# Performance work log

Hardware: AMD Instinct MI355X
Metric: run time of the kernel (lower is better)

## Reference

```python
import jax, jax.numpy as jnp
import numpy as np

WS = 8          # window_size
DISP = WS // 2  # cyclic shift displacement
HEADS = 12
HEAD_DIM = 32
SCALE = HEAD_DIM ** -0.5


def _rel_indices():
    # indices of (x, y) for x in range(WS) for y in range(WS)
    idx = np.stack(np.meshgrid(np.arange(WS), np.arange(WS), indexing='ij'), -1).reshape(-1, 2)
    return idx[None, :, :] - idx[:, None, :] + WS - 1  # (WS^2, WS^2, 2), values in [0, 2*WS-2]


def _masks():
    ninf = -np.inf
    # upper/lower mask: blocks attention across the vertical wrap boundary
    m_ul = np.zeros((WS * WS, WS * WS), np.float32)
    m_ul[-DISP * WS:, :-DISP * WS] = ninf
    m_ul[:-DISP * WS, -DISP * WS:] = ninf
    # left/right mask: blocks attention across the horizontal wrap boundary
    m4 = np.zeros((WS, WS, WS, WS), np.float32)  # (h1, w1, h2, w2)
    m4[:, -DISP:, :, :-DISP] = ninf
    m4[:, :-DISP, :, -DISP:] = ninf
    m_lr = m4.reshape(WS * WS, WS * WS)
    return jnp.asarray(m_ul), jnp.asarray(m_lr)


def setup_inputs() -> dict:
    key = jax.random.key(0)
    k1, k2, k3, k4, k5 = jax.random.split(key, 5)
    dim = HEADS * HEAD_DIM  # 384
    return {
        'x': jax.random.normal(k1, (16, 64, 64, dim), jnp.float32),
        'w_qkv': jax.random.normal(k2, (dim, 3 * dim), jnp.float32) * 0.02,
        'pos_embedding': jax.random.normal(k3, (2 * WS - 1, 2 * WS - 1), jnp.float32),
        'w_out': jax.random.normal(k4, (dim, dim), jnp.float32) * 0.02,
        'b_out': jax.random.normal(k5, (dim,), jnp.float32) * 0.02,
    }


def reference(x, w_qkv, pos_embedding, w_out, b_out):
    b, H, W, dim = x.shape
    nw_h, nw_w = H // WS, W // WS
    # cyclic shift
    x = jnp.roll(x, (-DISP, -DISP), axis=(1, 2))
    qkv = x @ w_qkv  # (b, H, W, 3*inner)

    def to_windows(t):
        # (b, H, W, inner) -> (b, heads, nw_h*nw_w, WS*WS, head_dim)
        t = t.reshape(b, nw_h, WS, nw_w, WS, HEADS, HEAD_DIM)
        return t.transpose(0, 5, 1, 3, 2, 4, 6).reshape(b, HEADS, nw_h * nw_w, WS * WS, HEAD_DIM)

    q, k, v = [to_windows(t) for t in jnp.split(qkv, 3, axis=-1)]
    dots = jnp.einsum('bhwid,bhwjd->bhwij', q, k) * SCALE

    rel = _rel_indices()
    dots = dots + pos_embedding[rel[..., 0], rel[..., 1]]  # relative position bias

    m_ul, m_lr = _masks()
    dots = dots.at[:, :, -nw_w:].add(m_ul)            # last row of windows
    dots = dots.at[:, :, nw_w - 1::nw_w].add(m_lr)    # last column of windows

    attn = jax.nn.softmax(dots, axis=-1)
    out = jnp.einsum('bhwij,bhwjd->bhwid', attn, v)
    # windows -> image layout
    out = out.reshape(b, HEADS, nw_h, nw_w, WS, WS, HEAD_DIM)
    out = out.transpose(0, 2, 4, 3, 5, 1, 6).reshape(b, H, W, HEADS * HEAD_DIM)
    out = out @ w_out + b_out
    # cyclic back shift
    return jnp.roll(out, (DISP, DISP), axis=(1, 2))
```

## Files before the change

### kernel.cpp

```cpp
#include <hip/hip_runtime.h>
#include <stdint.h>

#define HEADS 12
#define HD 32
#define DIM 384
#define NQKV 1152
#define NPIX 4096
#define NB 16

typedef __attribute__((ext_vector_type(8))) short bf16x8;
typedef __attribute__((ext_vector_type(4))) short bf16x4;
typedef __attribute__((ext_vector_type(4))) float f32x4;

__device__ __forceinline__ unsigned short f2bf(float f) {
  uint32_t u = __builtin_bit_cast(uint32_t, f);
  u += 0x7FFF + ((u >> 16) & 1);
  return (unsigned short)(u >> 16);
}

#define GL_LDS(gp, lp) __builtin_amdgcn_global_load_lds( \
    (const __attribute__((address_space(1))) void*)(gp),  \
    (__attribute__((address_space(3))) void*)(lp), 16, 0, 0)

__global__ void convert_all(const float* __restrict__ x,
                            const float* __restrict__ wqkv,
                            const float* __restrict__ wout,
                            unsigned short* __restrict__ xb,
                            unsigned short* __restrict__ wqkvT,
                            unsigned short* __restrict__ woutT) {
  int bid = blockIdx.x;
  if (bid < 12288) {
    int i = bid * 256 + threadIdx.x;
    const float4* xp = (const float4*)x;
    float4 a = xp[2 * i], b2 = xp[2 * i + 1];
    union { bf16x8 v; unsigned short s[8]; } u;
    u.s[0] = f2bf(a.x);  u.s[1] = f2bf(a.y);
    u.s[2] = f2bf(a.z);  u.s[3] = f2bf(a.w);
    u.s[4] = f2bf(b2.x); u.s[5] = f2bf(b2.y);
    u.s[6] = f2bf(b2.z); u.s[7] = f2bf(b2.w);
    ((bf16x8*)xb)[i] = u.v;
  } else {
    int tid = (bid - 12288) * 256 + threadIdx.x;
    if (tid < NQKV * DIM) {
      int n = tid / DIM, k = tid % DIM;
      wqkvT[tid] = f2bf(wqkv[(size_t)k * NQKV + n]);
    }
    if (tid < DIM * DIM) {
      int n = tid / DIM, k = tid % DIM;
      woutT[tid] = f2bf(wout[(size_t)k * DIM + n]);
    }
  }
}

__global__ __launch_bounds__(256, 4) void gemm_qkv(
    const unsigned short* __restrict__ xb,
    const unsigned short* __restrict__ wT,
    unsigned short* __restrict__ qkv)
{
  __shared__ unsigned short lA[128 * 64];
  __shared__ unsigned short lB[128 * 64];
  const int tid = threadIdx.x;
  const int wid = tid >> 6, lane = tid & 63;
  const int wr = wid >> 1, wc = wid & 1;
  const int lr = lane >> 4, lc = lane & 15;

  const int f = blockIdx.x;
  const int xcd = f & 7, idx = f >> 3;
  const int nt = idx % 9, mt = xcd * 64 + idx / 9;
  const int m0 = mt * 128, n0 = nt * 128;

  const int srow = wid * 32 + (lane >> 3);
  const int scol = ((lane & 7) ^ (lane >> 3)) * 8;
  const unsigned short* agp = xb + (size_t)(m0 + srow) * DIM + scol;
  const unsigned short* bgp = wT + (size_t)(n0 + srow) * DIM + scol;

  const f32x4 z4 = {0.f, 0.f, 0.f, 0.f};
  f32x4 acc[4][4];
#pragma unroll
  for (int i = 0; i < 4; i++)
#pragma unroll
    for (int j = 0; j < 4; j++) acc[i][j] = z4;

  auto stage = [&](int t) {
#pragma unroll
    for (int i = 0; i < 4; i++) {
      GL_LDS(agp + (size_t)(i * 8) * DIM + t * 64, &lA[(wid * 4 + i) * 512]);
      GL_LDS(bgp + (size_t)(i * 8) * DIM + t * 64, &lB[(wid * 4 + i) * 512]);
    }
  };
  auto compute = [&]() {
    const int sw = lc & 7;
#pragma unroll
    for (int kk = 0; kk < 2; kk++) {
      bf16x8 afr[4], bfr[4];
#pragma unroll
      for (int mi = 0; mi < 4; mi++)
        afr[mi] = *(const bf16x8*)&lA[(wr * 64 + mi * 16 + lc) * 64 + (((kk * 4 + lr) ^ sw) * 8)];
#pragma unroll
      for (int ni = 0; ni < 4; ni++)
        bfr[ni] = *(const bf16x8*)&lB[(wc * 64 + ni * 16 + lc) * 64 + (((kk * 4 + lr) ^ sw) * 8)];
#pragma unroll
      for (int mi = 0; mi < 4; mi++)
#pragma unroll
        for (int ni = 0; ni < 4; ni++)
          acc[mi][ni] = __builtin_amdgcn_mfma_f32_16x16x32_bf16(afr[mi], bfr[ni], acc[mi][ni], 0, 0, 0);
    }
  };

  for (int t = 0; t < 6; ++t) {
    stage(t);
    __syncthreads();
    compute();
    if (t < 5) __syncthreads();
  }

#pragma unroll
  for (int mi = 0; mi < 4; mi++) {
    int row = m0 + wr * 64 + mi * 16 + lr * 4;
#pragma unroll
    for (int reg = 0; reg < 4; reg++) {
      size_t rb = (size_t)(row + reg) * NQKV + n0 + wc * 64 + lc;
#pragma unroll
      for (int ni = 0; ni < 4; ni++)
        qkv[rb + ni * 16] = f2bf(acc[mi][ni][reg]);
    }
  }
}

__global__ __launch_bounds__(256) void attn_kernel(
    const unsigned short* __restrict__ qkv,
    const float* __restrict__ pos,
    unsigned short* __restrict__ Z)
{
  __shared__ float s_pos[225];
  __shared__ unsigned short Plds[4][64 * 80];
  __shared__ unsigned short Vt[4][32 * 80];

  if (threadIdx.x < 225) s_pos[threadIdx.x] = pos[threadIdx.x];

  const int wid = threadIdx.x >> 6, lane = threadIdx.x & 63;
  const int lr = lane >> 4, lc = lane & 15;
  const int task = blockIdx.x * 4 + wid;
  const int win = task & 63;
  const int head = (task >> 6) % HEADS;
  const int b = task / (HEADS * 64);
  const int wh = win >> 3, ww = win & 7;
  const bool ulm = (wh == 7), lrm = (ww == 7);

  auto pixof = [&](int t) {
    int hh = (wh * 8 + (t >> 3) + 4) & 63;
    int w2 = (ww * 8 + (t & 7) + 4) & 63;
    return hh * 64 + w2;
  };

  bf16x8 qf[4], kf[4];
  unsigned short* vt = &Vt[wid][0];
#pragma unroll
  for (int g = 0; g < 4; ++g) {
    int t = g * 16 + lc;
    const unsigned short* base =
        qkv + (size_t)(b * NPIX + pixof(t)) * NQKV + head * HD + lr * 8;
    qf[g] = *(const bf16x8*)(base);
    kf[g] = *(const bf16x8*)(base + DIM);
    union { bf16x8 v; unsigned short s[8]; } uv;
    uv.v = *(const bf16x8*)(base + 2 * DIM);
#pragma unroll
    for (int j = 0; j < 8; j++) vt[(lr * 8 + j) * 80 + t] = uv.s[j];
  }
  __syncthreads();

  const f32x4 z4 = {0.f, 0.f, 0.f, 0.f};
  f32x4 sacc[4][4];
#pragma unroll
  for (int i = 0; i < 4; i++)
#pragma unroll
    for (int j = 0; j < 4; j++) sacc[i][j] = z4;

#pragma unroll
  for (int mi = 0; mi < 4; mi++)
#pragma unroll
    for (int ni = 0; ni < 4; ni++)
      sacc[mi][ni] = __builtin_amdgcn_mfma_f32_16x16x32_bf16(qf[mi], kf[ni], sacc[mi][ni], 0, 0, 0);

  const float SC = 0.17677669529663687f;
#pragma unroll
  for (int mi = 0; mi < 4; mi++) {
#pragma unroll
    for (int reg = 0; reg < 4; reg++) {
      int i = mi * 16 + lr * 4 + reg;
      int xi = i >> 3, yi = i & 7;
#pragma unroll
      for (int ni = 0; ni < 4; ni++) {
        int j = ni * 16 + lc;
        int xj = j >> 3, yj = j & 7;
        float s = sacc[mi][ni][reg] * SC + s_pos[(xj - xi + 7) * 15 + (yj - yi + 7)];
        if (ulm && ((i >= 32) != (j >= 32))) s = -1e30f;
        if (lrm && ((yi >= 4) != (yj >= 4))) s = -1e30f;
        sacc[mi][ni][reg] = s;
      }
    }
  }

  float inv[4][4];
  unsigned short* pl = &Plds[wid][0];
#pragma unroll
  for (int mi = 0; mi < 4; mi++) {
#pragma unroll
    for (int reg = 0; reg < 4; reg++) {
      float m = fmaxf(fmaxf(sacc[mi][0][reg], sacc[mi][1][reg]),
                      fmaxf(sacc[mi][2][reg], sacc[mi][3][reg]));
      m = fmaxf(m, __shfl_xor(m, 1));
      m = fmaxf(m, __shfl_xor(m, 2));
      m = fmaxf(m, __shfl_xor(m, 4));
      m = fmaxf(m, __shfl_xor(m, 8));
      int i = mi * 16 + lr * 4 + reg;
      float sum = 0.f;
#pragma unroll
      for (int ni = 0; ni < 4; ni++) {
        float p = exp2f((sacc[mi][ni][reg] - m) * 1.44269504f);
        sum += p;
        pl[i * 80 + ni * 16 + lc] = f2bf(p);
      }
      sum += __shfl_xor(sum, 1);
      sum += __shfl_xor(sum, 2);
      sum += __shfl_xor(sum, 4);
      sum += __shfl_xor(sum, 8);
      inv[mi][reg] = 1.0f / sum;
    }
  }
  __syncthreads();

  f32x4 oacc[4][2];
#pragma unroll
  for (int i = 0; i < 4; i++) { oacc[i][0] = z4; oacc[i][1] = z4; }

#pragma unroll
  for (int kk = 0; kk < 2; kk++) {
    bf16x8 vfr[2];
#pragma unroll
    for (int ni = 0; ni < 2; ni++)
      vfr[ni] = *(const bf16x8*)&vt[(ni * 16 + lc) * 80 + kk * 32 + lr * 8];
#pragma unroll
    for (int mi = 0; mi < 4; mi++) {
      bf16x8 pf = *(const bf16x8*)&pl[(mi * 16 + lc) * 80 + kk * 32 + lr * 8];
#pragma unroll
      for (int ni = 0; ni < 2; ni++)
        oacc[mi][ni] = __builtin_amdgcn_mfma_f32_16x16x32_bf16(pf, vfr[ni], oacc[mi][ni], 0, 0, 0);
    }
  }

#pragma unroll
  for (int mi = 0; mi < 4; mi++) {
#pragma unroll
    for (int reg = 0; reg < 4; reg++) {
      int i = mi * 16 + lr * 4 + reg;
      size_t zb = ((size_t)b * NPIX + pixof(i)) * DIM + head * HD;
      float sc = inv[mi][reg];
#pragma unroll
      for (int ni = 0; ni < 2; ni++)
        Z[zb + ni * 16 + lc] = f2bf(oacc[mi][ni][reg] * sc);
    }
  }
}

__global__ __launch_bounds__(256, 4) void gemm_out(
    const unsigned short* __restrict__ Zb,
    const unsigned short* __restrict__ wT,
    const float* __restrict__ bout,
    float* __restrict__ out)
{
  __shared__ unsigned short lA[128 * 64];
  __shared__ unsigned short lB[128 * 64];
  const int tid = threadIdx.x;
  const int wid = tid >> 6, lane = tid & 63;
  const int wr = wid >> 1, wc = wid & 1;
  const int lr = lane >> 4, lc = lane & 15;

  const int f = blockIdx.x;
  const int xcd = f & 7, idx = f >> 3;
  const int nt = idx % 3, mt = xcd * 64 + idx / 3;
  const int m0 = mt * 128, n0 = nt * 128;

  const int srow = wid * 32 + (lane >> 3);
  const int scol = ((lane & 7) ^ (lane >> 3)) * 8;
  const unsigned short* agp = Zb + (size_t)(m0 + srow) * DIM + scol;
  const unsigned short* bgp = wT + (size_t)(n0 + srow) * DIM + scol;

  const f32x4 z4 = {0.f, 0.f, 0.f, 0.f};
  f32x4 acc[4][4];
#pragma unroll
  for (int i = 0; i < 4; i++)
#pragma unroll
    for (int j = 0; j < 4; j++) acc[i][j] = z4;

  auto stage = [&](int t) {
#pragma unroll
    for (int i = 0; i < 4; i++) {
      GL_LDS(agp + (size_t)(i * 8) * DIM + t * 64, &lA[(wid * 4 + i) * 512]);
      GL_LDS(bgp + (size_t)(i * 8) * DIM + t * 64, &lB[(wid * 4 + i) * 512]);
    }
  };
  auto compute = [&]() {
    const int sw = lc & 7;
#pragma unroll
    for (int kk = 0; kk < 2; kk++) {
      bf16x8 afr[4], bfr[4];
#pragma unroll
      for (int mi = 0; mi < 4; mi++)
        afr[mi] = *(const bf16x8*)&lA[(wr * 64 + mi * 16 + lc) * 64 + (((kk * 4 + lr) ^ sw) * 8)];
#pragma unroll
      for (int ni = 0; ni < 4; ni++)
        bfr[ni] = *(const bf16x8*)&lB[(wc * 64 + ni * 16 + lc) * 64 + (((kk * 4 + lr) ^ sw) * 8)];
#pragma unroll
      for (int mi = 0; mi < 4; mi++)
#pragma unroll
        for (int ni = 0; ni < 4; ni++)
          acc[mi][ni] = __builtin_amdgcn_mfma_f32_16x16x32_bf16(afr[mi], bfr[ni], acc[mi][ni], 0, 0, 0);
    }
  };

  for (int t = 0; t < 6; ++t) {
    stage(t);
    __syncthreads();
    compute();
    if (t < 5) __syncthreads();
  }

  float bo[4];
#pragma unroll
  for (int ni = 0; ni < 4; ni++) bo[ni] = bout[n0 + wc * 64 + ni * 16 + lc];

#pragma unroll
  for (int mi = 0; mi < 4; mi++) {
    int row = m0 + wr * 64 + mi * 16 + lr * 4;
#pragma unroll
    for (int reg = 0; reg < 4; reg++) {
      size_t rb = (size_t)(row + reg) * DIM + n0 + wc * 64 + lc;
#pragma unroll
      for (int ni = 0; ni < 4; ni++)
        out[rb + ni * 16] = acc[mi][ni][reg] + bo[ni];
    }
  }
}

extern "C" void kernel_launch(void* const* d_in, const int* in_sizes, int n_in,
                              void* d_out, int out_size, void* d_ws, size_t ws_size,
                              hipStream_t stream) {
  const float* x    = (const float*)d_in[0];
  const float* wqkv = (const float*)d_in[1];
  const float* pos  = (const float*)d_in[2];
  const float* wout = (const float*)d_in[3];
  const float* bout = (const float*)d_in[4];
  float* out = (float*)d_out;

  char* ws = (char*)d_ws;
  unsigned short* wqkvT = (unsigned short*)ws;
  unsigned short* woutT = (unsigned short*)(ws + 884736);
  unsigned short* qkv   = (unsigned short*)(ws + 1179648);
  unsigned short* xb    = (unsigned short*)(ws + 1179648 + 150994944);
  unsigned short* Zb    = xb;

  convert_all<<<14016, 256, 0, stream>>>(x, wqkv, wout, xb, wqkvT, woutT);
  gemm_qkv<<<4608, 256, 0, stream>>>(xb, wqkvT, qkv);
  attn_kernel<<<3072, 256, 0, stream>>>(qkv, pos, Zb);
  gemm_out<<<1536, 256, 0, stream>>>(Zb, woutT, bout, out);
}
```

Baseline: 192.9 us.

## Precompute bias/mask table and keep softmax probabilities in registers via transposed QK

Adds a precomputed table of four variants (64x64 each) of relative-position bias plus shift masks, built in the convert kernel and stored temporarily in the output buffer. The attention kernel loads bias rows directly instead of computing indices and masks per element. It computes S^T = K·Q^T so each lane's probabilities can be normalized, packed to bf16 and reshuffled with ds_bpermute into MFMA operand layout. This removes the P round-trip through LDS and both barriers. V^T in LDS gets an XOR swizzle to reduce bank conflicts. It relies on gemm_out overwriting the table region later and adds cross-lane permute traffic.

```diff
diff --git a/kernel.cpp b/kernel.cpp
--- a/kernel.cpp
+++ b/kernel.cpp
@@ -25,9 +25,11 @@
 __global__ void convert_all(const float* __restrict__ x,
                             const float* __restrict__ wqkv,
                             const float* __restrict__ wout,
+                            const float* __restrict__ pos,
                             unsigned short* __restrict__ xb,
                             unsigned short* __restrict__ wqkvT,
-                            unsigned short* __restrict__ woutT) {
+                            unsigned short* __restrict__ woutT,
+                            float* __restrict__ tab) {
   int bid = blockIdx.x;
   if (bid < 12288) {
     int i = bid * 256 + threadIdx.x;
@@ -39,7 +41,7 @@
     u.s[4] = f2bf(b2.x); u.s[5] = f2bf(b2.y);
     u.s[6] = f2bf(b2.z); u.s[7] = f2bf(b2.w);
     ((bf16x8*)xb)[i] = u.v;
-  } else {
+  } else if (bid < 14016) {
     int tid = (bid - 12288) * 256 + threadIdx.x;
     if (tid < NQKV * DIM) {
       int n = tid / DIM, k = tid % DIM;
@@ -49,6 +51,15 @@
       int n = tid / DIM, k = tid % DIM;
       woutT[tid] = f2bf(wout[(size_t)k * DIM + n]);
     }
+  } else {
+    int tid = (bid - 14016) * 256 + threadIdx.x;
+    int v = tid >> 12, rem = tid & 4095;
+    int i = rem >> 6, j = rem & 63;
+    int xi = i >> 3, yi = i & 7, xj = j >> 3, yj = j & 7;
+    float val = pos[(xj - xi + 7) * 15 + (yj - yi + 7)];
+    if ((v & 1) && ((i >= 32) != (j >= 32))) val = -1e30f;
+    if ((v & 2) && ((yi >= 4) != (yj >= 4))) val = -1e30f;
+    tab[tid] = val;
   }
 }
 
@@ -129,14 +140,10 @@
 
 __global__ __launch_bounds__(256) void attn_kernel(
     const unsigned short* __restrict__ qkv,
-    const float* __restrict__ pos,
+    const float* __restrict__ tab,
     unsigned short* __restrict__ Z)
 {
-  __shared__ float s_pos[225];
-  __shared__ unsigned short Plds[4][64 * 80];
   __shared__ unsigned short Vt[4][32 * 80];
-
-  if (threadIdx.x < 225) s_pos[threadIdx.x] = pos[threadIdx.x];
 
   const int wid = threadIdx.x >> 6, lane = threadIdx.x & 63;
   const int lr = lane >> 4, lc = lane & 15;
@@ -145,7 +152,7 @@
   const int head = (task >> 6) % HEADS;
   const int b = task / (HEADS * 64);
   const int wh = win >> 3, ww = win & 7;
-  const bool ulm = (wh == 7), lrm = (ww == 7);
+  const float* tv = tab + (((wh == 7) ? 1 : 0) + ((ww == 7) ? 2 : 0)) * 4096;
 
   auto pixof = [&](int t) {
     int hh = (wh * 8 + (t >> 3) + 4) & 63;
@@ -153,8 +160,8 @@
     return hh * 64 + w2;
   };
 
+  unsigned short* vt = &Vt[wid][0];
   bf16x8 qf[4], kf[4];
-  unsigned short* vt = &Vt[wid][0];
 #pragma unroll
   for (int g = 0; g < 4; ++g) {
     int t = g * 16 + lc;
@@ -165,70 +172,77 @@
     union { bf16x8 v; unsigned short s[8]; } uv;
     uv.v = *(const bf16x8*)(base + 2 * DIM);
 #pragma unroll
-    for (int j = 0; j < 8; j++) vt[(lr * 8 + j) * 80 + t] = uv.s[j];
-  }
-  __syncthreads();
-
+    for (int j = 0; j < 8; j++) {
+      int row = lr * 8 + j;
+      int addr = row * 80 + (((g * 2 + (lc >> 3)) ^ ((row >> 2) & 3)) << 3) + (lc & 7);
+      vt[addr] = uv.s[j];
+    }
+  }
+
+  const float SC = 0.17677669529663687f;
   const f32x4 z4 = {0.f, 0.f, 0.f, 0.f};
-  f32x4 sacc[4][4];
-#pragma unroll
-  for (int i = 0; i < 4; i++)
-#pragma unroll
-    for (int j = 0; j < 4; j++) sacc[i][j] = z4;
-
-#pragma unroll
-  for (int mi = 0; mi < 4; mi++)
-#pragma unroll
-    for (int ni = 0; ni < 4; ni++)
-      sacc[mi][ni] = __builtin_amdgcn_mfma_f32_16x16x32_bf16(qf[mi], kf[ni], sacc[mi][ni], 0, 0, 0);
-
-  const float SC = 0.17677669529663687f;
-#pragma unroll
-  for (int mi = 0; mi < 4; mi++) {
-#pragma unroll
-    for (int reg = 0; reg < 4; reg++) {
-      int i = mi * 16 + lr * 4 + reg;
-      int xi = i >> 3, yi = i & 7;
-#pragma unroll
-      for (int ni = 0; ni < 4; ni++) {
-        int j = ni * 16 + lc;
-        int xj = j >> 3, yj = j & 7;
-        float s = sacc[mi][ni][reg] * SC + s_pos[(xj - xi + 7) * 15 + (yj - yi + 7)];
-        if (ulm && ((i >= 32) != (j >= 32))) s = -1e30f;
-        if (lrm && ((yi >= 4) != (yj >= 4))) s = -1e30f;
-        sacc[mi][ni][reg] = s;
+  uint32_t pf[4][2][4];
+  const int srcA = (lc + 16 * (2 * (lr & 1))) << 2;
+  const int srcB = srcA + 64;
+  const bool hiSel = (lr >> 1) != 0;
+
+#pragma unroll
+  for (int bq = 0; bq < 4; bq++) {
+    f32x4 tb[4];
+#pragma unroll
+    for (int a = 0; a < 4; a++)
+      tb[a] = *(const f32x4*)&tv[(bq * 16 + lc) * 64 + a * 16 + lr * 4];
+    f32x4 s[4];
+#pragma unroll
+    for (int a = 0; a < 4; a++)
+      s[a] = __builtin_amdgcn_mfma_f32_16x16x32_bf16(kf[a], qf[bq], z4, 0, 0, 0);
+
+    float m = -3.0e38f;
+#pragma unroll
+    for (int a = 0; a < 4; a++)
+#pragma unroll
+      for (int r = 0; r < 4; r++) {
+        float val = s[a][r] * SC + tb[a][r];
+        s[a][r] = val;
+        m = fmaxf(m, val);
       }
-    }
-  }
-
-  float inv[4][4];
-  unsigned short* pl = &Plds[wid][0];
-#pragma unroll
-  for (int mi = 0; mi < 4; mi++) {
-#pragma unroll
-    for (int reg = 0; reg < 4; reg++) {
-      float m = fmaxf(fmaxf(sacc[mi][0][reg], sacc[mi][1][reg]),
-                      fmaxf(sacc[mi][2][reg], sacc[mi][3][reg]));
-      m = fmaxf(m, __shfl_xor(m, 1));
-      m = fmaxf(m, __shfl_xor(m, 2));
-      m = fmaxf(m, __shfl_xor(m, 4));
-      m = fmaxf(m, __shfl_xor(m, 8));
-      int i = mi * 16 + lr * 4 + reg;
-      float sum = 0.f;
-#pragma unroll
-      for (int ni = 0; ni < 4; ni++) {
-        float p = exp2f((sacc[mi][ni][reg] - m) * 1.44269504f);
+    m = fmaxf(m, __shfl_xor(m, 16));
+    m = fmaxf(m, __shfl_xor(m, 32));
+    float sum = 0.f;
+#pragma unroll
+    for (int a = 0; a < 4; a++)
+#pragma unroll
+      for (int r = 0; r < 4; r++) {
+        float p = exp2f((s[a][r] - m) * 1.44269504f);
+        s[a][r] = p;
         sum += p;
-        pl[i * 80 + ni * 16 + lc] = f2bf(p);
       }
-      sum += __shfl_xor(sum, 1);
-      sum += __shfl_xor(sum, 2);
-      sum += __shfl_xor(sum, 4);
-      sum += __shfl_xor(sum, 8);
-      inv[mi][reg] = 1.0f / sum;
-    }
-  }
-  __syncthreads();
+    sum += __shfl_xor(sum, 16);
+    sum += __shfl_xor(sum, 32);
+    float iv = 1.0f / sum;
+
+    uint32_t pk[4][2];
+#pragma unroll
+    for (int a = 0; a < 4; a++)
+#pragma unroll
+      for (int w = 0; w < 2; w++) {
+        float plo = s[a][2 * w] * iv, phi = s[a][2 * w + 1] * iv;
+        uint32_t r;
+        asm("v_cvt_pk_bf16_f32 %0, %1, %2" : "=v"(r) : "v"(plo), "v"(phi));
+        pk[a][w] = r;
+      }
+#pragma unroll
+    for (int kk = 0; kk < 2; kk++)
+#pragma unroll
+      for (int wp = 0; wp < 4; wp++) {
+        int sa = (wp >> 1) ? srcB : srcA;
+        uint32_t lo = (uint32_t)__builtin_amdgcn_ds_bpermute(sa, (int)pk[2 * kk][wp & 1]);
+        uint32_t hi = (uint32_t)__builtin_amdgcn_ds_bpermute(sa, (int)pk[2 * kk + 1][wp & 1]);
+        pf[bq][kk][wp] = hiSel ? hi : lo;
+      }
+  }
+
+  asm volatile("s_waitcnt lgkmcnt(0)" ::: "memory");
 
   f32x4 oacc[4][2];
 #pragma unroll
@@ -238,14 +252,19 @@
   for (int kk = 0; kk < 2; kk++) {
     bf16x8 vfr[2];
 #pragma unroll
-    for (int ni = 0; ni < 2; ni++)
-      vfr[ni] = *(const bf16x8*)&vt[(ni * 16 + lc) * 80 + kk * 32 + lr * 8];
+    for (int dt = 0; dt < 2; dt++) {
+      int rowd = dt * 16 + lc;
+      int addr = rowd * 80 + ((((kk * 4 + lr) ^ (lc >> 2)) & 7) << 3);
+      vfr[dt] = *(const bf16x8*)&vt[addr];
+    }
 #pragma unroll
     for (int mi = 0; mi < 4; mi++) {
-      bf16x8 pf = *(const bf16x8*)&pl[(mi * 16 + lc) * 80 + kk * 32 + lr * 8];
-#pragma unroll
-      for (int ni = 0; ni < 2; ni++)
-        oacc[mi][ni] = __builtin_amdgcn_mfma_f32_16x16x32_bf16(pf, vfr[ni], oacc[mi][ni], 0, 0, 0);
+      union { uint32_t u[4]; bf16x8 v; } pu;
+      pu.u[0] = pf[mi][kk][0]; pu.u[1] = pf[mi][kk][1];
+      pu.u[2] = pf[mi][kk][2]; pu.u[3] = pf[mi][kk][3];
+#pragma unroll
+      for (int dt = 0; dt < 2; dt++)
+        oacc[mi][dt] = __builtin_amdgcn_mfma_f32_16x16x32_bf16(pu.v, vfr[dt], oacc[mi][dt], 0, 0, 0);
     }
   }
 
@@ -255,10 +274,9 @@
     for (int reg = 0; reg < 4; reg++) {
       int i = mi * 16 + lr * 4 + reg;
       size_t zb = ((size_t)b * NPIX + pixof(i)) * DIM + head * HD;
-      float sc = inv[mi][reg];
-#pragma unroll
-      for (int ni = 0; ni < 2; ni++)
-        Z[zb + ni * 16 + lc] = f2bf(oacc[mi][ni][reg] * sc);
+#pragma unroll
+      for (int dt = 0; dt < 2; dt++)
+        Z[zb + dt * 16 + lc] = f2bf(oacc[mi][dt][reg]);
     }
   }
 }
@@ -359,9 +377,10 @@
   unsigned short* qkv   = (unsigned short*)(ws + 1179648);
   unsigned short* xb    = (unsigned short*)(ws + 1179648 + 150994944);
   unsigned short* Zb    = xb;
-
-  convert_all<<<14016, 256, 0, stream>>>(x, wqkv, wout, xb, wqkvT, woutT);
+  float* tab = out;
+
+  convert_all<<<14080, 256, 0, stream>>>(x, wqkv, wout, pos, xb, wqkvT, woutT, tab);
   gemm_qkv<<<4608, 256, 0, stream>>>(xb, wqkvT, qkv);
-  attn_kernel<<<3072, 256, 0, stream>>>(qkv, pos, Zb);
+  attn_kernel<<<3072, 256, 0, stream>>>(qkv, tab, Zb);
   gemm_out<<<1536, 256, 0, stream>>>(Zb, woutT, bout, out);
 }
```

After: 179.0 us. 1.08x faster.
